# Performance work log

Hardware: AMD Instinct MI355X
Metric: run time of the kernel (lower is better)

## Reference

```python
import jax, jax.numpy as jnp
import numpy as np

N = 50000        # nodes
E = 300000       # edges
D_IN = 256
D_H = 256
D_OUT = 64       # num classes
L = 3            # num GAT layers
G = 500          # num graphs in batch
NEG_SLOPE = 0.2


def setup_inputs() -> dict:
    key = jax.random.key(0)
    ks = jax.random.split(key, 12)
    x = jax.random.normal(ks[0], (N, D_IN), dtype=jnp.float32)
    edge_index = jax.random.randint(ks[1], (2, E), 0, N, dtype=jnp.int64)
    batch = jnp.sort(jax.random.randint(ks[2], (N,), 0, G, dtype=jnp.int64))
    # GAT layer params (all layers same width since D_IN == D_H)
    Ws = jax.random.normal(ks[3], (L, D_H, D_H), dtype=jnp.float32) * 0.05
    atts = jax.random.normal(ks[4], (L, 2 * D_H, 1), dtype=jnp.float32) * 0.05
    bs = jnp.zeros((L, D_H), dtype=jnp.float32)
    # post_mp: Linear(D_H,D_H) -> Dropout(0) -> Linear(D_H,D_OUT)
    pW1 = jax.random.normal(ks[5], (D_H, D_H), dtype=jnp.float32) * 0.05
    pb1 = jnp.zeros((D_H,), dtype=jnp.float32)
    pW2 = jax.random.normal(ks[6], (D_OUT, D_H), dtype=jnp.float32) * 0.05
    pb2 = jnp.zeros((D_OUT,), dtype=jnp.float32)
    return dict(x=x, edge_index=edge_index, batch=batch, Ws=Ws, atts=atts,
                bs=bs, pW1=pW1, pb1=pb1, pW2=pW2, pb2=pb2)


def _gat_layer(x, W, att, b, src, dst):
    h = x @ W.T                                   # [N, D_H] (lin, no bias)
    xi = h[dst]                                   # target features  [E, D_H]
    xj = h[src]                                   # source features  [E, D_H]
    e = jnp.concatenate([xi, xj], axis=1) @ att   # [E, 1]
    e = jax.nn.leaky_relu(e[:, 0], NEG_SLOPE)     # [E]
    # segment softmax keyed by destination node
    m = jax.ops.segment_max(e, dst, num_segments=N)
    m = jnp.where(jnp.isfinite(m), m, 0.0)        # empty segments -> 0
    ee = jnp.exp(e - m[dst])
    s = jax.ops.segment_sum(ee, dst, num_segments=N)
    alpha = ee / (s[dst] + 1e-16)                 # [E]
    # weighted scatter-add aggregation (aggr='add'); heads=1, concat view is identity
    out = jax.ops.segment_sum(alpha[:, None] * xj, dst, num_segments=N)
    return out + b


def reference(x, edge_index, batch, Ws, atts, bs, pW1, pb1, pW2, pb2):
    src = edge_index[0]
    dst = edge_index[1]
    for l in range(L):
        x = _gat_layer(x, Ws[l], atts[l], bs[l], src, dst)
    # Dropout(p=0) is identity
    x = jax.nn.relu(x)
    g = jax.ops.segment_max(x, batch, num_segments=G)   # global_max_pool [G, D_H]
    h = g @ pW1.T + pb1
    out = h @ pW2.T + pb2
    return jax.nn.log_softmax(out, axis=1)
```

## Files before the change

### kernel.cpp

```cpp
#include <hip/hip_runtime.h>
#include <math.h>

#define NEG_SLOPE 0.2f

typedef __attribute__((ext_vector_type(8))) short s16x8;
typedef __attribute__((ext_vector_type(4))) float f32x4;
typedef unsigned short ushort_t;
typedef unsigned int uint_t;

__device__ inline ushort_t f2bf(float f) {
    unsigned u = __float_as_uint(f);
    unsigned r = (u + 0x7fff + ((u >> 16) & 1)) >> 16;
    return (ushort_t)r;
}
__device__ inline float bf2f(ushort_t u) {
    return __uint_as_float(((unsigned)u) << 16);
}

__global__ __launch_bounds__(256) void cvt2_kernel(const float* __restrict__ a,
        ushort_t* __restrict__ oa, int na4,
        const float* __restrict__ b, ushort_t* __restrict__ ob, int nb4) {
    int i = blockIdx.x * 256 + threadIdx.x;
    if (i < na4) {
        float4 v = ((const float4*)a)[i];
        ushort4 o;
        o.x = f2bf(v.x); o.y = f2bf(v.y); o.z = f2bf(v.z); o.w = f2bf(v.w);
        ((ushort4*)oa)[i] = o;
    } else if (i - na4 < nb4) {
        int k = i - na4;
        float4 v = ((const float4*)b)[k];
        ushort4 o;
        o.x = f2bf(v.x); o.y = f2bf(v.y); o.z = f2bf(v.z); o.w = f2bf(v.w);
        ((ushort4*)ob)[k] = o;
    }
}

__global__ void deg_kernel(const int* __restrict__ ei, int* __restrict__ deg, int E) {
    int e = blockIdx.x * blockDim.x + threadIdx.x;
    if (e < E) atomicAdd(&deg[ei[E + e]], 1);
}

__global__ __launch_bounds__(1024) void scan1(const int* __restrict__ deg,
        int* __restrict__ tscan, int* __restrict__ bsum, int n) {
    __shared__ int ws[16];
    int t = threadIdx.x;
    int gi = blockIdx.x * 1024 + t;
    int v = (gi < n) ? deg[gi] : 0;
    int lane = t & 63, w = t >> 6;
    int s = v;
#pragma unroll
    for (int off = 1; off < 64; off <<= 1) {
        int u = __shfl_up(s, off);
        if (lane >= off) s += u;
    }
    if (lane == 63) ws[w] = s;
    __syncthreads();
    if (w == 0) {
        int x = (lane < 16) ? ws[lane] : 0;
#pragma unroll
        for (int off = 1; off < 16; off <<= 1) {
            int u = __shfl_up(x, off);
            if (lane >= off) x += u;
        }
        if (lane < 16) ws[lane] = x;
    }
    __syncthreads();
    int woff = (w > 0) ? ws[w - 1] : 0;
    if (gi < n) tscan[gi] = woff + s - v;
    if (t == 1023) bsum[blockIdx.x] = woff + s;
}

__global__ __launch_bounds__(1024) void scan3(const int* __restrict__ tscan,
        const int* __restrict__ bsum, const int* __restrict__ deg,
        int* __restrict__ rowptr, int* __restrict__ cursor, int n, int nb) {
    __shared__ int sboff;
    int t = threadIdx.x;
    if (t < 64) {
        int v = (t < nb) ? bsum[t] : 0;
        int s = v;
#pragma unroll
        for (int off = 1; off < 64; off <<= 1) {
            int u = __shfl_up(s, off);
            if (t >= off) s += u;
        }
        if (t == (int)blockIdx.x) sboff = s - v;
    }
    __syncthreads();
    int i = blockIdx.x * 1024 + t;
    if (i < n) {
        int v = tscan[i] + sboff;
        rowptr[i] = v;
        cursor[i] = v;
        if (i == n - 1) rowptr[n] = v + deg[i];
    }
}

__global__ void scatter_kernel(const int* __restrict__ ei, int* __restrict__ cursor,
                               int* __restrict__ adj, int E) {
    int e = blockIdx.x * blockDim.x + threadIdx.x;
    if (e < E) {
        int d = ei[E + e];
        int pos = atomicAdd(&cursor[d], 1);
        adj[pos] = ei[e];
    }
}

__global__ __launch_bounds__(256) void gemm_bf16(const ushort_t* __restrict__ A,
        const ushort_t* __restrict__ B, ushort_t* __restrict__ C,
        const float* __restrict__ att, float* __restrict__ a_dst,
        float* __restrict__ a_src, int n) {
    __shared__ ushort_t As[128 * 32];
    __shared__ ushort_t Bs[128 * 32];
    const int t = threadIdx.x;
    const int lane = t & 63, wid = t >> 6;
    const int wr = wid >> 1, wc = wid & 1;
    const long brow = (long)blockIdx.x * 128;
    const int bcol = blockIdx.y * 128;

    f32x4 acc[4][4] = {};

    const int r0 = wid * 16 + (lane >> 2);
    const int kof = (lane & 3) * 8;
    const int fr = lane & 15, kg = lane >> 4;

    for (int kt = 0; kt < 256; kt += 32) {
        __builtin_amdgcn_global_load_lds(
            (const __attribute__((address_space(1))) void*)(A + (brow + r0) * 256 + kt + kof),
            (__attribute__((address_space(3))) void*)(As + wid * 512 + lane * 8), 16, 0, 0);
        __builtin_amdgcn_global_load_lds(
            (const __attribute__((address_space(1))) void*)(A + (brow + r0 + 64) * 256 + kt + kof),
            (__attribute__((address_space(3))) void*)(As + (wid + 4) * 512 + lane * 8), 16, 0, 0);
        __builtin_amdgcn_global_load_lds(
            (const __attribute__((address_space(1))) void*)(B + (bcol + r0) * 256 + kt + kof),
            (__attribute__((address_space(3))) void*)(Bs + wid * 512 + lane * 8), 16, 0, 0);
        __builtin_amdgcn_global_load_lds(
            (const __attribute__((address_space(1))) void*)(B + (bcol + r0 + 64) * 256 + kt + kof),
            (__attribute__((address_space(3))) void*)(Bs + (wid + 4) * 512 + lane * 8), 16, 0, 0);
        asm volatile("s_waitcnt vmcnt(0)" ::: "memory");
        __syncthreads();

        s16x8 a[4], b[4];
#pragma unroll
        for (int m = 0; m < 4; m++)
            a[m] = *(const s16x8*)(As + (wr * 64 + m * 16 + fr) * 32 + kg * 8);
#pragma unroll
        for (int nn = 0; nn < 4; nn++)
            b[nn] = *(const s16x8*)(Bs + (wc * 64 + nn * 16 + fr) * 32 + kg * 8);
#pragma unroll
        for (int m = 0; m < 4; m++)
#pragma unroll
            for (int nn = 0; nn < 4; nn++)
                acc[m][nn] = __builtin_amdgcn_mfma_f32_16x16x32_bf16(a[m], b[nn], acc[m][nn], 0, 0, 0);
        __syncthreads();
    }

    const int rg = lane >> 4;
    const float* attL = att;
    const float* attR = att + 256;
#pragma unroll
    for (int m = 0; m < 4; m++) {
        long rbase = brow + wr * 64 + m * 16 + rg * 4;
#pragma unroll
        for (int r = 0; r < 4; r++) {
            long row = rbase + r;
            float sL = 0.f, sR = 0.f;
#pragma unroll
            for (int nn = 0; nn < 4; nn++) {
                int col = bcol + wc * 64 + nn * 16 + fr;
                float v = acc[m][nn][r];
                C[row * 256 + col] = f2bf(v);
                sL = fmaf(v, attL[col], sL);
                sR = fmaf(v, attR[col], sR);
            }
#pragma unroll
            for (int off = 8; off; off >>= 1) {
                sL += __shfl_xor(sL, off);
                sR += __shfl_xor(sR, off);
            }
            if (fr == 0 && row < n) {
                atomicAdd(&a_dst[row], sL);
                atomicAdd(&a_src[row], sR);
            }
        }
    }
}

__global__ __launch_bounds__(256) void gat_agg(const ushort_t* __restrict__ H,
        const float* __restrict__ a_dst, const float* __restrict__ a_src,
        const int* __restrict__ rowptr, const int* __restrict__ adj,
        const float* __restrict__ bias, ushort_t* __restrict__ OUTbf, int n) {
    int w = threadIdx.x >> 6, lane = threadIdx.x & 63;
    int node = blockIdx.x * 4 + w;
    if (node >= n) return;
    int beg = rowptr[node], end = rowptr[node + 1];
    int degree = end - beg;
    float ai = a_dst[node];

    const int g = lane >> 4, fl = lane & 15;
    float ssum = 0.f;
    float acc[16];
#pragma unroll
    for (int k = 0; k < 16; k++) acc[k] = 0.f;
    float m;

    if (degree <= 64) {
        int sidx_c = 0;
        float e_c = -3.4e38f;
        if (lane < degree) {
            sidx_c = adj[beg + lane];
            float tt = ai + a_src[sidx_c];
            e_c = (tt > 0.f) ? tt : NEG_SLOPE * tt;
        }
        m = e_c;
#pragma unroll
        for (int off = 32; off; off >>= 1) m = fmaxf(m, __shfl_xor(m, off));

        for (int j0 = 0; j0 < degree; j0 += 4) {
            int j = j0 + g;
            if (j < degree) {
                float ej = __shfl(e_c, j);
                int sj = __shfl(sidx_c, j);
                float wgt = expf(ej - m);
                ssum += wgt;
                const ushort_t* hp = H + (size_t)sj * 256 + fl * 16;
                uint4 q0 = *(const uint4*)(hp);
                uint4 q1 = *(const uint4*)(hp + 8);
                uint_t qs[8] = {q0.x, q0.y, q0.z, q0.w, q1.x, q1.y, q1.z, q1.w};
#pragma unroll
                for (int k = 0; k < 8; k++) {
                    float flo = __uint_as_float(qs[k] << 16);
                    float fhi = __uint_as_float(qs[k] & 0xffff0000u);
                    acc[2 * k]     = fmaf(wgt, flo, acc[2 * k]);
                    acc[2 * k + 1] = fmaf(wgt, fhi, acc[2 * k + 1]);
                }
            }
        }
    } else {
        m = -3.4e38f;
        for (int j = beg + lane; j < end; j += 64) {
            float e = ai + a_src[adj[j]];
            e = (e > 0.f) ? e : NEG_SLOPE * e;
            m = fmaxf(m, e);
        }
#pragma unroll
        for (int off = 32; off; off >>= 1) m = fmaxf(m, __shfl_xor(m, off));

        for (int j0 = beg; j0 < end; j0 += 4) {
            int j = j0 + g;
            if (j < end) {
                int sidx = adj[j];
                float tt = ai + a_src[sidx];
                tt = (tt > 0.f) ? tt : NEG_SLOPE * tt;
                float wgt = expf(tt - m);
                ssum += wgt;
                const ushort_t* hp = H + (size_t)sidx * 256 + fl * 16;
                uint4 q0 = *(const uint4*)(hp);
                uint4 q1 = *(const uint4*)(hp + 8);
                uint_t qs[8] = {q0.x, q0.y, q0.z, q0.w, q1.x, q1.y, q1.z, q1.w};
#pragma unroll
                for (int k = 0; k < 8; k++) {
                    float flo = __uint_as_float(qs[k] << 16);
                    float fhi = __uint_as_float(qs[k] & 0xffff0000u);
                    acc[2 * k]     = fmaf(wgt, flo, acc[2 * k]);
                    acc[2 * k + 1] = fmaf(wgt, fhi, acc[2 * k + 1]);
                }
            }
        }
    }

#pragma unroll
    for (int k = 0; k < 16; k++) {
        acc[k] += __shfl_xor(acc[k], 16);
        acc[k] += __shfl_xor(acc[k], 32);
    }
    ssum += __shfl_xor(ssum, 16);
    ssum += __shfl_xor(ssum, 32);

    if (g == 0) {
        float inv = 1.f / (ssum + 1e-16f);
        float bv[16];
        *(float4*)&bv[0]  = *(const float4*)(bias + fl * 16);
        *(float4*)&bv[4]  = *(const float4*)(bias + fl * 16 + 4);
        *(float4*)&bv[8]  = *(const float4*)(bias + fl * 16 + 8);
        *(float4*)&bv[12] = *(const float4*)(bias + fl * 16 + 12);
        uint_t ou[8];
#pragma unroll
        for (int k = 0; k < 8; k++) {
            uint_t lo = f2bf(acc[2 * k] * inv + bv[2 * k]);
            uint_t hi = f2bf(acc[2 * k + 1] * inv + bv[2 * k + 1]);
            ou[k] = lo | (hi << 16);
        }
        uint4* op = (uint4*)(OUTbf + (size_t)node * 256 + fl * 16);
        op[0] = make_uint4(ou[0], ou[1], ou[2], ou[3]);
        op[1] = make_uint4(ou[4], ou[5], ou[6], ou[7]);
    }
}

__global__ __launch_bounds__(1024) void pool_kernel(const ushort_t* __restrict__ X,
        const int* __restrict__ batch, float* __restrict__ gbuf, int n) {
    __shared__ float red[4][256];
    int g = blockIdx.x;
    int c = threadIdx.x & 255;
    int rg = threadIdx.x >> 8;
    int lo = 0, hi = n;
    while (lo < hi) { int mid = (lo + hi) >> 1; if (batch[mid] < g) lo = mid + 1; else hi = mid; }
    int start = lo;
    hi = n;
    while (lo < hi) { int mid = (lo + hi) >> 1; if (batch[mid] < g + 1) lo = mid + 1; else hi = mid; }
    int end_ = lo;
    float m = 0.f;
    for (int i = start + rg; i < end_; i += 4)
        m = fmaxf(m, bf2f(X[(size_t)i * 256 + c]));
    red[rg][c] = m;
    __syncthreads();
    if (rg == 0) {
        m = fmaxf(fmaxf(red[0][c], red[1][c]), fmaxf(red[2][c], red[3][c]));
        gbuf[g * 256 + c] = m;
    }
}

__global__ __launch_bounds__(256) void final_kernel(const float* __restrict__ gbuf,
        const float* __restrict__ pW1, const float* __restrict__ pb1,
        const float* __restrict__ pW2, const float* __restrict__ pb2,
        float* __restrict__ out) {
    __shared__ float gl[256];
    __shared__ float h1[256];
    int g = blockIdx.x, t = threadIdx.x;
    gl[t] = gbuf[g * 256 + t];
    __syncthreads();
    float acc = pb1[t];
    for (int k = 0; k < 256; k++) acc = fmaf(gl[k], pW1[t * 256 + k], acc);
    h1[t] = acc;
    __syncthreads();
    if (t < 64) {
        float o = pb2[t];
        for (int k = 0; k < 256; k++) o = fmaf(h1[k], pW2[t * 256 + k], o);
        float mx = o;
#pragma unroll
        for (int off = 32; off; off >>= 1) mx = fmaxf(mx, __shfl_xor(mx, off));
        float ex = expf(o - mx);
        float s = ex;
#pragma unroll
        for (int off = 32; off; off >>= 1) s += __shfl_xor(s, off);
        out[g * 64 + t] = o - mx - logf(s);
    }
}

extern "C" void kernel_launch(void* const* d_in, const int* in_sizes, int n_in,
                              void* d_out, int out_size, void* d_ws, size_t ws_size,
                              hipStream_t stream) {
    const float* x     = (const float*)d_in[0];
    const int*   ei    = (const int*)d_in[1];
    const int*   batch = (const int*)d_in[2];
    const float* Ws    = (const float*)d_in[3];
    const float* atts  = (const float*)d_in[4];
    const float* bs    = (const float*)d_in[5];
    const float* pW1   = (const float*)d_in[6];
    const float* pb1   = (const float*)d_in[7];
    const float* pW2   = (const float*)d_in[8];
    const float* pb2   = (const float*)d_in[9];
    float* out = (float*)d_out;

    const int N = in_sizes[0] / 256;
    const int E = in_sizes[1] / 2;
    const int G = out_size / 64;
    const int L = in_sizes[3] / (256 * 256);
    const int MB = (N + 127) / 128;
    const int Npad = MB * 128;
    const int NT = (N + 1023) / 1024;

    char* ws = (char*)d_ws;
    size_t off = 0;
    auto alloc = [&](size_t bytes) -> char* {
        char* p = ws + off;
        off += (bytes + 255) & ~size_t(255);
        return p;
    };
    ushort_t* Hbf    = (ushort_t*)alloc((size_t)Npad * 256 * 2);
    ushort_t* Xbf    = (ushort_t*)alloc((size_t)Npad * 256 * 2);
    ushort_t* Wbf    = (ushort_t*)alloc((size_t)L * 256 * 256 * 2);
    char*     zbeg   = ws + off;
    int*      deg    = (int*)alloc((size_t)N * 4);
    float*    a_all  = (float*)alloc((size_t)L * 2 * N * 4);
    size_t    zlen   = (size_t)((ws + off) - zbeg);
    int*      rowptr = (int*)alloc((size_t)(N + 1) * 4);
    int*      cursor = (int*)alloc((size_t)N * 4);
    int*      adj    = (int*)alloc((size_t)E * 4);
    int*      tscan  = (int*)alloc((size_t)N * 4);
    int*      bsum   = (int*)alloc((size_t)64 * 4);
    float*    gbuf   = (float*)alloc((size_t)G * 256 * 4);

    hipMemsetAsync(zbeg, 0, zlen, stream);

    int eb = (E + 255) / 256;
    deg_kernel<<<eb, 256, 0, stream>>>(ei, deg, E);
    scan1<<<NT, 1024, 0, stream>>>(deg, tscan, bsum, N);
    scan3<<<NT, 1024, 0, stream>>>(tscan, bsum, deg, rowptr, cursor, N, NT);
    scatter_kernel<<<eb, 256, 0, stream>>>(ei, cursor, adj, E);

    int na4 = N * 64, nb4 = L * 16384;
    cvt2_kernel<<<(na4 + nb4 + 255) / 256, 256, 0, stream>>>(x, Xbf, na4, Ws, Wbf, nb4);

    for (int l = 0; l < L; ++l) {
        float* a_dst = a_all + (size_t)l * 2 * N;
        float* a_src = a_dst + N;
        dim3 ggrid(MB, 2);
        gemm_bf16<<<ggrid, 256, 0, stream>>>(Xbf, Wbf + (size_t)l * 65536, Hbf,
                                             atts + (size_t)l * 512, a_dst, a_src, N);
        gat_agg<<<(N + 3) / 4, 256, 0, stream>>>(Hbf, a_dst, a_src, rowptr, adj,
                                                 bs + (size_t)l * 256, Xbf, N);
    }
    pool_kernel<<<G, 1024, 0, stream>>>(Xbf, batch, gbuf, N);
    final_kernel<<<G, 256, 0, stream>>>(gbuf, pW1, pb1, pW2, pb2, out);
}
```

Measured before the change: 351.6 us.

## Fuse CSR build into cooperative kernel, drop atomics and memset, merge pool+final

The four CSR-construction launches and the memset are replaced by a single cooperative kernel that uses grid-wide syncs between the degree, scan and scatter phases. The GEMM epilogue now reduces the attention dot products across column-half waves in shared memory and writes per-column-block partials, so the float atomics and the zeroed buffer are gone. The aggregation kernel sums the two partials on read. Pool and final MLP are merged into one kernel, which removes launches and an intermediate buffer but adds extra reads in gat_agg and depends on grid.sync behaving correctly with 49 blocks of 1024 threads.

```diff
diff --git a/kernel.cpp b/kernel.cpp
--- a/kernel.cpp
+++ b/kernel.cpp
@@ -1,5 +1,8 @@
 #include <hip/hip_runtime.h>
+#include <hip/hip_cooperative_groups.h>
 #include <math.h>
+
+namespace cg = cooperative_groups;
 
 #define NEG_SLOPE 0.2f
 
@@ -35,16 +38,21 @@
     }
 }
 
-__global__ void deg_kernel(const int* __restrict__ ei, int* __restrict__ deg, int E) {
-    int e = blockIdx.x * blockDim.x + threadIdx.x;
-    if (e < E) atomicAdd(&deg[ei[E + e]], 1);
-}
-
-__global__ __launch_bounds__(1024) void scan1(const int* __restrict__ deg,
-        int* __restrict__ tscan, int* __restrict__ bsum, int n) {
+__global__ __launch_bounds__(1024) void csr_coop(const int* __restrict__ ei,
+        int* __restrict__ deg, int* __restrict__ rowptr, int* __restrict__ cursor,
+        int* __restrict__ adj, int* __restrict__ bsum, int E, int n) {
+    cg::grid_group grid = cg::this_grid();
+    const int t = threadIdx.x, b = blockIdx.x;
+    const int gt = b * 1024 + t, GT = gridDim.x * 1024;
+
+    for (int i = gt; i < n; i += GT) deg[i] = 0;
+    grid.sync();
+
+    for (int e = gt; e < E; e += GT) atomicAdd(&deg[ei[E + e]], 1);
+    grid.sync();
+
     __shared__ int ws[16];
-    int t = threadIdx.x;
-    int gi = blockIdx.x * 1024 + t;
+    const int gi = gt;
     int v = (gi < n) ? deg[gi] : 0;
     int lane = t & 63, w = t >> 6;
     int s = v;
@@ -66,39 +74,31 @@
     }
     __syncthreads();
     int woff = (w > 0) ? ws[w - 1] : 0;
-    if (gi < n) tscan[gi] = woff + s - v;
-    if (t == 1023) bsum[blockIdx.x] = woff + s;
-}
-
-__global__ __launch_bounds__(1024) void scan3(const int* __restrict__ tscan,
-        const int* __restrict__ bsum, const int* __restrict__ deg,
-        int* __restrict__ rowptr, int* __restrict__ cursor, int n, int nb) {
+    if (gi < n) rowptr[gi] = woff + s - v;
+    if (t == 1023) bsum[b] = woff + s;
+    grid.sync();
+
     __shared__ int sboff;
-    int t = threadIdx.x;
     if (t < 64) {
-        int v = (t < nb) ? bsum[t] : 0;
-        int s = v;
+        int vv = (t < (int)gridDim.x) ? bsum[t] : 0;
+        int ss = vv;
 #pragma unroll
         for (int off = 1; off < 64; off <<= 1) {
-            int u = __shfl_up(s, off);
-            if (t >= off) s += u;
-        }
-        if (t == (int)blockIdx.x) sboff = s - v;
-    }
-    __syncthreads();
-    int i = blockIdx.x * 1024 + t;
-    if (i < n) {
-        int v = tscan[i] + sboff;
-        rowptr[i] = v;
-        cursor[i] = v;
-        if (i == n - 1) rowptr[n] = v + deg[i];
-    }
-}
-
-__global__ void scatter_kernel(const int* __restrict__ ei, int* __restrict__ cursor,
-                               int* __restrict__ adj, int E) {
-    int e = blockIdx.x * blockDim.x + threadIdx.x;
-    if (e < E) {
+            int u = __shfl_up(ss, off);
+            if (t >= off) ss += u;
+        }
+        if (t == b) sboff = ss - vv;
+    }
+    __syncthreads();
+    if (gi < n) {
+        int r = rowptr[gi] + sboff;
+        rowptr[gi] = r;
+        cursor[gi] = r;
+        if (gi == n - 1) rowptr[n] = r + deg[gi];
+    }
+    grid.sync();
+
+    for (int e = gt; e < E; e += GT) {
         int d = ei[E + e];
         int pos = atomicAdd(&cursor[d], 1);
         adj[pos] = ei[e];
@@ -107,10 +107,11 @@
 
 __global__ __launch_bounds__(256) void gemm_bf16(const ushort_t* __restrict__ A,
         const ushort_t* __restrict__ B, ushort_t* __restrict__ C,
-        const float* __restrict__ att, float* __restrict__ a_dst,
-        float* __restrict__ a_src, int n) {
+        const float* __restrict__ att, float* __restrict__ a_part, int n) {
     __shared__ ushort_t As[128 * 32];
     __shared__ ushort_t Bs[128 * 32];
+    __shared__ float redL[2][128];
+    __shared__ float redR[2][128];
     const int t = threadIdx.x;
     const int lane = t & 63, wid = t >> 6;
     const int wr = wid >> 1, wc = wid & 1;
@@ -177,16 +178,27 @@
                 sL += __shfl_xor(sL, off);
                 sR += __shfl_xor(sR, off);
             }
-            if (fr == 0 && row < n) {
-                atomicAdd(&a_dst[row], sL);
-                atomicAdd(&a_src[row], sR);
+            if (fr == 0) {
+                int rl = wr * 64 + m * 16 + rg * 4 + r;
+                redL[wc][rl] = sL;
+                redR[wc][rl] = sR;
             }
         }
     }
+    __syncthreads();
+    if (t < 128) {
+        long row = brow + t;
+        if (row < n) {
+            float* aL = a_part + (size_t)blockIdx.y * n;
+            float* aR = a_part + 2 * (size_t)n + (size_t)blockIdx.y * n;
+            aL[row] = redL[0][t] + redL[1][t];
+            aR[row] = redR[0][t] + redR[1][t];
+        }
+    }
 }
 
 __global__ __launch_bounds__(256) void gat_agg(const ushort_t* __restrict__ H,
-        const float* __restrict__ a_dst, const float* __restrict__ a_src,
+        const float* __restrict__ a_part,
         const int* __restrict__ rowptr, const int* __restrict__ adj,
         const float* __restrict__ bias, ushort_t* __restrict__ OUTbf, int n) {
     int w = threadIdx.x >> 6, lane = threadIdx.x & 63;
@@ -194,7 +206,11 @@
     if (node >= n) return;
     int beg = rowptr[node], end = rowptr[node + 1];
     int degree = end - beg;
-    float ai = a_dst[node];
+    const float* aL0 = a_part;
+    const float* aL1 = a_part + n;
+    const float* aR0 = a_part + 2 * (size_t)n;
+    const float* aR1 = a_part + 3 * (size_t)n;
+    float ai = aL0[node] + aL1[node];
 
     const int g = lane >> 4, fl = lane & 15;
     float ssum = 0.f;
@@ -208,7 +224,7 @@
         float e_c = -3.4e38f;
         if (lane < degree) {
             sidx_c = adj[beg + lane];
-            float tt = ai + a_src[sidx_c];
+            float tt = ai + aR0[sidx_c] + aR1[sidx_c];
             e_c = (tt > 0.f) ? tt : NEG_SLOPE * tt;
         }
         m = e_c;
@@ -238,7 +254,8 @@
     } else {
         m = -3.4e38f;
         for (int j = beg + lane; j < end; j += 64) {
-            float e = ai + a_src[adj[j]];
+            int s = adj[j];
+            float e = ai + aR0[s] + aR1[s];
             e = (e > 0.f) ? e : NEG_SLOPE * e;
             m = fmaxf(m, e);
         }
@@ -249,7 +266,7 @@
             int j = j0 + g;
             if (j < end) {
                 int sidx = adj[j];
-                float tt = ai + a_src[sidx];
+                float tt = ai + aR0[sidx] + aR1[sidx];
                 tt = (tt > 0.f) ? tt : NEG_SLOPE * tt;
                 float wgt = expf(tt - m);
                 ssum += wgt;
@@ -296,12 +313,18 @@
     }
 }
 
-__global__ __launch_bounds__(1024) void pool_kernel(const ushort_t* __restrict__ X,
-        const int* __restrict__ batch, float* __restrict__ gbuf, int n) {
+__global__ __launch_bounds__(1024) void poolfinal_kernel(const ushort_t* __restrict__ X,
+        const int* __restrict__ batch,
+        const float* __restrict__ pW1, const float* __restrict__ pb1,
+        const float* __restrict__ pW2, const float* __restrict__ pb2,
+        float* __restrict__ out, int n) {
     __shared__ float red[4][256];
+    __shared__ float gl[256];
+    __shared__ float h1[256];
     int g = blockIdx.x;
-    int c = threadIdx.x & 255;
-    int rg = threadIdx.x >> 8;
+    int t = threadIdx.x;
+    int c = t & 255;
+    int rg = t >> 8;
     int lo = 0, hi = n;
     while (lo < hi) { int mid = (lo + hi) >> 1; if (batch[mid] < g) lo = mid + 1; else hi = mid; }
     int start = lo;
@@ -313,24 +336,14 @@
         m = fmaxf(m, bf2f(X[(size_t)i * 256 + c]));
     red[rg][c] = m;
     __syncthreads();
-    if (rg == 0) {
-        m = fmaxf(fmaxf(red[0][c], red[1][c]), fmaxf(red[2][c], red[3][c]));
-        gbuf[g * 256 + c] = m;
-    }
-}
-
-__global__ __launch_bounds__(256) void final_kernel(const float* __restrict__ gbuf,
-        const float* __restrict__ pW1, const float* __restrict__ pb1,
-        const float* __restrict__ pW2, const float* __restrict__ pb2,
-        float* __restrict__ out) {
-    __shared__ float gl[256];
-    __shared__ float h1[256];
-    int g = blockIdx.x, t = threadIdx.x;
-    gl[t] = gbuf[g * 256 + t];
-    __syncthreads();
-    float acc = pb1[t];
-    for (int k = 0; k < 256; k++) acc = fmaf(gl[k], pW1[t * 256 + k], acc);
-    h1[t] = acc;
+    if (rg == 0)
+        gl[c] = fmaxf(fmaxf(red[0][c], red[1][c]), fmaxf(red[2][c], red[3][c]));
+    __syncthreads();
+    if (t < 256) {
+        float acc = pb1[t];
+        for (int k = 0; k < 256; k++) acc = fmaf(gl[k], pW1[t * 256 + k], acc);
+        h1[t] = acc;
+    }
     __syncthreads();
     if (t < 64) {
         float o = pb2[t];
@@ -379,37 +392,32 @@
     ushort_t* Hbf    = (ushort_t*)alloc((size_t)Npad * 256 * 2);
     ushort_t* Xbf    = (ushort_t*)alloc((size_t)Npad * 256 * 2);
     ushort_t* Wbf    = (ushort_t*)alloc((size_t)L * 256 * 256 * 2);
-    char*     zbeg   = ws + off;
+    float*    a_part = (float*)alloc((size_t)4 * N * 4);
     int*      deg    = (int*)alloc((size_t)N * 4);
-    float*    a_all  = (float*)alloc((size_t)L * 2 * N * 4);
-    size_t    zlen   = (size_t)((ws + off) - zbeg);
     int*      rowptr = (int*)alloc((size_t)(N + 1) * 4);
     int*      cursor = (int*)alloc((size_t)N * 4);
     int*      adj    = (int*)alloc((size_t)E * 4);
-    int*      tscan  = (int*)alloc((size_t)N * 4);
     int*      bsum   = (int*)alloc((size_t)64 * 4);
-    float*    gbuf   = (float*)alloc((size_t)G * 256 * 4);
-
-    hipMemsetAsync(zbeg, 0, zlen, stream);
-
-    int eb = (E + 255) / 256;
-    deg_kernel<<<eb, 256, 0, stream>>>(ei, deg, E);
-    scan1<<<NT, 1024, 0, stream>>>(deg, tscan, bsum, N);
-    scan3<<<NT, 1024, 0, stream>>>(tscan, bsum, deg, rowptr, cursor, N, NT);
-    scatter_kernel<<<eb, 256, 0, stream>>>(ei, cursor, adj, E);
+
+    {
+        int E_ = E, N_ = N;
+        const int* ei_ = ei;
+        int *deg_ = deg, *rowptr_ = rowptr, *cursor_ = cursor, *adj_ = adj, *bsum_ = bsum;
+        void* cargs[] = {(void*)&ei_, (void*)&deg_, (void*)&rowptr_, (void*)&cursor_,
+                         (void*)&adj_, (void*)&bsum_, (void*)&E_, (void*)&N_};
+        hipLaunchCooperativeKernel((const void*)csr_coop, dim3(NT), dim3(1024),
+                                   cargs, 0, stream);
+    }
 
     int na4 = N * 64, nb4 = L * 16384;
     cvt2_kernel<<<(na4 + nb4 + 255) / 256, 256, 0, stream>>>(x, Xbf, na4, Ws, Wbf, nb4);
 
     for (int l = 0; l < L; ++l) {
-        float* a_dst = a_all + (size_t)l * 2 * N;
-        float* a_src = a_dst + N;
         dim3 ggrid(MB, 2);
         gemm_bf16<<<ggrid, 256, 0, stream>>>(Xbf, Wbf + (size_t)l * 65536, Hbf,
-                                             atts + (size_t)l * 512, a_dst, a_src, N);
-        gat_agg<<<(N + 3) / 4, 256, 0, stream>>>(Hbf, a_dst, a_src, rowptr, adj,
+                                             atts + (size_t)l * 512, a_part, N);
+        gat_agg<<<(N + 3) / 4, 256, 0, stream>>>(Hbf, a_part, rowptr, adj,
                                                  bs + (size_t)l * 256, Xbf, N);
     }
-    pool_kernel<<<G, 1024, 0, stream>>>(Xbf, batch, gbuf, N);
-    final_kernel<<<G, 256, 0, stream>>>(gbuf, pW1, pb1, pW2, pb2, out);
-}
+    poolfinal_kernel<<<G, 1024, 0, stream>>>(Xbf, batch, pW1, pb1, pW2, pb2, out, N);
+}
```

Result: slower. 402.8 us (+14.6%).
